# Performance work log

Measured on AMD Instinct MI355X. Metric: run time of the kernel, lower is better.

The kernel has to match this reference:

```python
import jax, jax.numpy as jnp
import numpy as np

H = 16      # num_attention_heads
D = 128     # head_size
ROT = 32    # rotary_ndims
WIN = 256   # attention_window[layer_id]
G = 64      # max_global_tokens
BASE = 10000.0


def _rotate_half(x):
    x1, x2 = jnp.split(x, 2, axis=-1)
    return jnp.concatenate([-x2, x1], axis=-1)


def setup_inputs() -> dict:
    key = jax.random.key(0)
    ks = jax.random.split(key, 6)
    B, S, HD = 2, 2048, H * D
    hidden_states = jax.random.normal(ks[0], (B, S, HD), jnp.float32)
    attention_mask = jnp.zeros((B, 1, 1, S), jnp.float32)
    glob_idx = jnp.sort(jax.random.randint(ks[1], (B, G), 0, S), axis=-1)
    W_qkv = jax.random.normal(ks[2], (HD, 3 * HD), jnp.float32) * 0.02
    b_qkv = jnp.zeros((3 * HD,), jnp.float32)
    W_o = jax.random.normal(ks[3], (HD, HD), jnp.float32) * 0.02
    b_o = jnp.zeros((HD,), jnp.float32)
    return {"hidden_states": hidden_states, "attention_mask": attention_mask,
            "glob_idx": glob_idx, "W_qkv": W_qkv, "b_qkv": b_qkv,
            "W_o": W_o, "b_o": b_o}


def reference(hidden_states, attention_mask, glob_idx, W_qkv, b_qkv, W_o, b_o):
    B, S, HD = hidden_states.shape
    qkv = (hidden_states @ W_qkv + b_qkv).reshape(B, S, H, 3 * D)
    q = qkv[..., :D].transpose(0, 2, 1, 3)        # [B,H,S,D]
    k = qkv[..., D:2 * D].transpose(0, 2, 1, 3)
    v = qkv[..., 2 * D:].transpose(0, 2, 1, 3)

    # GPT-NeoX rotary on first ROT dims
    inv_freq = 1.0 / (BASE ** (jnp.arange(0, ROT, 2, dtype=jnp.float32) / ROT))
    freqs = jnp.einsum('s,f->sf', jnp.arange(S, dtype=jnp.float32), inv_freq)
    emb = jnp.concatenate([freqs, freqs], axis=-1)           # [S,ROT]
    cos = jnp.cos(emb)[None, None]
    sin = jnp.sin(emb)[None, None]
    q = jnp.concatenate([q[..., :ROT] * cos + _rotate_half(q[..., :ROT]) * sin,
                         q[..., ROT:]], axis=-1)
    k = jnp.concatenate([k[..., :ROT] * cos + _rotate_half(k[..., :ROT]) * sin,
                         k[..., ROT:]], axis=-1)

    # step_attn path: keys/values are head-averaged before attention (key.mean(1))
    k_mean = k.mean(axis=1)   # [B,S,D]
    v_mean = v.mean(axis=1)
    scale = 1.0 / jnp.sqrt(jnp.float32(D))
    minv = jnp.finfo(jnp.float32).min

    s0 = jnp.einsum('bhqd,bkd->bhqk', q[:, :, :WIN], k_mean[:, :WIN]) * scale
    causal = jnp.tril(jnp.ones((WIN, WIN), bool))
    s0 = jnp.where(causal[None, None], s0, minv) + attention_mask[..., :WIN]
    out0 = jnp.einsum('bhqk,bkd->bhqd', jax.nn.softmax(s0, axis=-1), v_mean[:, :WIN])

    Sq = S - WIN
    steps = jnp.arange(Sq)
    win_pos = steps[:, None] + 1 + jnp.arange(WIN)[None, :]
    k_win = k_mean[:, win_pos]
    v_win = v_mean[:, win_pos]
    mask_win = attention_mask[:, 0, 0, :][:, win_pos][:, None]
    qs = q[:, :, WIN:]                                        # [B,H,Sq,D]
    s_win = jnp.einsum('bhqd,bqwd->bhqw', qs, k_win) * scale + mask_win

    k_glob = jnp.take_along_axis(k_mean, glob_idx[..., None], axis=1)  # [B,G,D]
    v_glob = jnp.take_along_axis(v_mean, glob_idx[..., None], axis=1)
    # sorted indices: 'filter < i then truncate to G' == prefix-valid mask per slot
    valid = (glob_idx[:, None, :] < steps[None, :, None])[:, None]     # [B,1,Sq,G]
    s_glob = jnp.where(valid, jnp.einsum('bhqd,bgd->bhqg', qs, k_glob) * scale, minv)

    w = jax.nn.softmax(jnp.concatenate([s_glob, s_win], axis=-1), axis=-1)
    out_steps = (jnp.einsum('bhqg,bgd->bhqd', w[..., :G], v_glob)
                 + jnp.einsum('bhqw,bqwd->bhqd', w[..., G:], v_win))

    out = jnp.concatenate([out0, out_steps], axis=2)          # [B,H,S,D]
    out = out.transpose(0, 2, 1, 3).reshape(B, S, HD)
    return out @ W_o + b_o
```

## Files before the change

### kernel.cpp

```cpp
#include <hip/hip_runtime.h>
#include <math.h>

#define SCALE_ 0.08838834764831845f
#define MINV_  (-3.4028234663852886e38f)

typedef __bf16 bf16;
typedef bf16  bf16x4 __attribute__((ext_vector_type(4)));
typedef bf16  bf16x8 __attribute__((ext_vector_type(8)));
typedef float f32x4  __attribute__((ext_vector_type(4)));
typedef float f32x16 __attribute__((ext_vector_type(16)));
typedef float float4v __attribute__((ext_vector_type(4)));

#define LD8(p) (*(const bf16x8*)(p))

__device__ __forceinline__ f32x4 mfma16(bf16x8 a, bf16x8 b, f32x4 c) {
    return __builtin_amdgcn_mfma_f32_16x16x32_bf16(a, b, c, 0, 0, 0);
}
__device__ __forceinline__ f32x16 mfma32(bf16x8 a, bf16x8 b, f32x16 c) {
    return __builtin_amdgcn_mfma_f32_32x32x16_bf16(a, b, c, 0, 0, 0);
}

typedef const __attribute__((address_space(1))) void* gas_t;
typedef __attribute__((address_space(3))) void* sas_t;
__device__ __forceinline__ void gload_lds16(const void* g, void* l) {
    __builtin_amdgcn_global_load_lds((gas_t)g, (sas_t)l, 16, 0, 0);
}


__global__ __launch_bounds__(256) void cast_hidden_kernel(const float* __restrict__ X, bf16* __restrict__ Y)
{
    int i = (blockIdx.x * 256 + threadIdx.x) * 4;
    float4v v = *(const float4v*)(X + i);
    bf16x4 o; o.x = (bf16)v.x; o.y = (bf16)v.y; o.z = (bf16)v.z; o.w = (bf16)v.w;
    *(bf16x4*)(Y + i) = o;
}

__global__ __launch_bounds__(256) void transpose_cast_kernel(const float* __restrict__ W, bf16* __restrict__ BT,
                                                             int srcStride, int qmap)
{
    __shared__ float tile[32][33];
    int k0 = blockIdx.x * 32, n0 = blockIdx.y * 32;
    int c = threadIdx.x & 31, r = threadIdx.x >> 5;
    int n = n0 + c;
    int src = qmap ? ((n >> 7) * 384 + (n & 127)) : n;
    #pragma unroll
    for (int rr = 0; rr < 32; rr += 8)
        tile[r + rr][c] = W[(size_t)(k0 + r + rr) * srcStride + src];
    __syncthreads();
    #pragma unroll
    for (int rr = 0; rr < 32; rr += 8)
        BT[(size_t)(n0 + r + rr) * 2048 + k0 + c] = (bf16)tile[c][r + rr];
}

__global__ __launch_bounds__(256) void bt1_kv_kernel(const float* __restrict__ Wqkv, bf16* __restrict__ BT1)
{
    int k0 = blockIdx.x * 16;
    int j = threadIdx.x;
    float acc[16];
    #pragma unroll
    for (int k = 0; k < 16; k++) acc[k] = 0.f;
    for (int h = 0; h < 16; h++) {
        #pragma unroll
        for (int k = 0; k < 16; k++)
            acc[k] += Wqkv[(size_t)(k0 + k) * 6144 + h * 384 + 128 + j];
    }
    #pragma unroll
    for (int k = 0; k < 16; k++)
        BT1[(size_t)(2048 + j) * 2048 + k0 + k] = (bf16)(acc[k] * 0.0625f);
}

__global__ void bias1_kernel(const float* __restrict__ bqkv, float* __restrict__ bias1)
{
    int c = blockIdx.x * 256 + threadIdx.x;
    if (c >= 2304) return;
    if (c < 2048) bias1[c] = bqkv[(c >> 7) * 384 + (c & 127)];
    else {
        int j = c - 2048; float s = 0.f;
        for (int h = 0; h < 16; h++) s += bqkv[h * 384 + 128 + j];
        bias1[c] = s * 0.0625f;
    }
}

template<int OUT_BF16>
__global__ __launch_bounds__(256) void gemm_kernel(const bf16* __restrict__ A, const bf16* __restrict__ BT,
                                                   const float* __restrict__ bias, void* __restrict__ Cout,
                                                   int M, int N, int K)
{
    __shared__ __align__(16) bf16 As[128 * 64];
    __shared__ __align__(16) bf16 Bs[128 * 64];
    const int tid  = threadIdx.x;
    const int wv   = tid >> 6, lane = tid & 63, l32 = lane & 31, half = lane >> 5;
    const int wrow = wv >> 1, wcol = wv & 1;
    const int m0 = blockIdx.y * 128, n0 = blockIdx.x * 128;

    int rowS[4], colS[4];
    #pragma unroll
    for (int j = 0; j < 4; j++) {
        int flat = (wv * 4 + j) * 64 + lane;
        int row = flat >> 3, cp = flat & 7;
        rowS[j] = row;
        colS[j] = (cp ^ (row & 7)) * 8;
    }

    f32x16 acc[2][2];
    #pragma unroll
    for (int i = 0; i < 2; i++)
        #pragma unroll
        for (int j = 0; j < 2; j++)
            #pragma unroll
            for (int r = 0; r < 16; r++) acc[i][j][r] = 0.f;

    for (int kk = 0; kk < K; kk += 64) {
        __syncthreads();
        #pragma unroll
        for (int j = 0; j < 4; j++) {
            gload_lds16(A  + (size_t)(m0 + rowS[j]) * K + kk + colS[j], &As[(wv * 4 + j) * 512]);
            gload_lds16(BT + (size_t)(n0 + rowS[j]) * K + kk + colS[j], &Bs[(wv * 4 + j) * 512]);
        }
        __syncthreads();

        bf16x8 af[2][4], bfr[2][4];
        #pragma unroll
        for (int mt = 0; mt < 2; mt++) {
            int row = wrow * 64 + mt * 32 + l32;
            #pragma unroll
            for (int k16 = 0; k16 < 4; k16++) {
                int lc = k16 * 2 + half;
                af[mt][k16] = LD8(&As[row * 64 + ((lc ^ (row & 7)) * 8)]);
            }
        }
        #pragma unroll
        for (int nt = 0; nt < 2; nt++) {
            int row = wcol * 64 + nt * 32 + l32;
            #pragma unroll
            for (int k16 = 0; k16 < 4; k16++) {
                int lc = k16 * 2 + half;
                bfr[nt][k16] = LD8(&Bs[row * 64 + ((lc ^ (row & 7)) * 8)]);
            }
        }
        #pragma unroll
        for (int k16 = 0; k16 < 4; k16++)
            #pragma unroll
            for (int mt = 0; mt < 2; mt++)
                #pragma unroll
                for (int nt = 0; nt < 2; nt++)
                    acc[mt][nt] = mfma32(af[mt][k16], bfr[nt][k16], acc[mt][nt]);
    }

    #pragma unroll
    for (int mt = 0; mt < 2; mt++) {
        #pragma unroll
        for (int nt = 0; nt < 2; nt++) {
            int n = n0 + wcol * 64 + nt * 32 + l32;
            float bn = bias[n];
            #pragma unroll
            for (int r = 0; r < 16; r++) {
                int m = m0 + wrow * 64 + mt * 32 + (r & 3) + 8 * (r >> 2) + 4 * half;
                float v = acc[mt][nt][r] + bn;
                if (OUT_BF16) ((bf16*)Cout)[(size_t)m * N + n] = (bf16)v;
                else          ((float*)Cout)[(size_t)m * N + n] = v;
            }
        }
    }
}

__global__ __launch_bounds__(320) void rotary_kernel(bf16* __restrict__ C1)
{
    int row = blockIdx.x;
    int s = row & 2047;
    int t = threadIdx.x;
    if (t >= 272) return;
    int g = t >> 4, dd = t & 15;
    bf16* ptr = C1 + (size_t)row * 2304 + (g < 16 ? g * 128 : 2048);
    float x0 = (float)ptr[dd], x1 = (float)ptr[dd + 16];
    const float L = 0.575646273248511f;
    float inv = __expf(-L * (float)dd);
    float ang = (float)s * inv;
    float c, si;
    __sincosf(ang, &si, &c);
    ptr[dd]      = (bf16)(x0 * c - x1 * si);
    ptr[dd + 16] = (bf16)(x1 * c + x0 * si);
}

__global__ __launch_bounds__(256) void build_vmT_kernel(const bf16* __restrict__ C1, bf16* __restrict__ vmT)
{
    __shared__ float tile[32][33];
    int b = blockIdx.z;
    int s0 = blockIdx.x * 32, d0 = blockIdx.y * 32;
    int c = threadIdx.x & 31, r = threadIdx.x >> 5;
    #pragma unroll
    for (int rr = 0; rr < 32; rr += 8)
        tile[r + rr][c] = (float)C1[(size_t)(b * 2048 + s0 + r + rr) * 2304 + 2176 + d0 + c];
    __syncthreads();
    #pragma unroll
    for (int rr = 0; rr < 32; rr += 8)
        vmT[(size_t)(b * 128 + d0 + r + rr) * 2048 + s0 + c] = (bf16)tile[c][r + rr];
}

__global__ __launch_bounds__(256) void pretile_kernel(const bf16* __restrict__ C1, const bf16* __restrict__ vmT,
                                                      const int* __restrict__ gidx,
                                                      bf16* __restrict__ KF, bf16* __restrict__ VF)
{
    int c = blockIdx.x, b = blockIdx.y;
    bool isGlob = (c == 32);
    for (int i = 0; i < 8; i++) {
        int sid = threadIdx.x + i * 256;
        int lane = sid & 63, fi = (sid >> 6) & 15;
        int l16 = lane & 15, quad = lane >> 4;
        if (sid < 1024) {
            int t = fi >> 2, ks = fi & 3;
            int pos = isGlob ? gidx[b * 64 + t * 16 + l16] : (c * 64 + t * 16 + l16);
            const bf16* src = C1 + (size_t)(b * 2048 + pos) * 2304 + 2048 + ks * 32 + quad * 8;
            *(bf16x8*)&KF[((size_t)(b * 33 + c) * 16 + fi) * 512 + lane * 8] = LD8(src);
        } else {
            int dt = fi >> 1, ks2 = fi & 1;
            int d = dt * 16 + l16;
            if (isGlob) {
                bf16 tmp[8];
                #pragma unroll
                for (int j = 0; j < 8; j++) {
                    int pos = gidx[b * 64 + ks2 * 32 + quad * 8 + j];
                    tmp[j] = vmT[(size_t)(b * 128 + d) * 2048 + pos];
                }
                #pragma unroll
                for (int j = 0; j < 8; j++)
                    VF[((size_t)(b * 33 + 32) * 16 + fi) * 512 + lane * 8 + j] = tmp[j];
            } else {
                const bf16* src = vmT + (size_t)(b * 128 + d) * 2048 + c * 64 + ks2 * 32 + quad * 8;
                *(bf16x8*)&VF[((size_t)(b * 33 + c) * 16 + fi) * 512 + lane * 8] = LD8(src);
            }
        }
    }
}

#define PSTRIDE 88

__global__ __launch_bounds__(256) void attn0_kernel(const bf16* __restrict__ C1, const bf16* __restrict__ KF,
                                                    const bf16* __restrict__ VF, const float* __restrict__ mask,
                                                    bf16* __restrict__ attn)
{
    const int bx = blockIdx.x, h = blockIdx.y, b = blockIdx.z;
    const int tid = threadIdx.x, wv = tid >> 6, lane = tid & 63, quad = lane >> 4, l16 = lane & 15;
    const int q0 = (bx * 4 + wv) * 16;

    __shared__ __align__(16) bf16 Ps[4 * 16 * PSTRIDE];
    bf16* Pw = &Ps[wv * (16 * PSTRIDE)];

    bf16x8 af[4];
    const bf16* qbase = C1 + (size_t)(b * 2048 + q0 + l16) * 2304 + h * 128;
    #pragma unroll
    for (int ks = 0; ks < 4; ks++) af[ks] = LD8(qbase + ks * 32 + quad * 8);

    f32x4 m_run = (f32x4){MINV_, MINV_, MINV_, MINV_};
    f32x4 l_run = (f32x4){0.f, 0.f, 0.f, 0.f};
    f32x4 O[8];
    #pragma unroll
    for (int dt = 0; dt < 8; dt++) O[dt] = (f32x4){0.f, 0.f, 0.f, 0.f};

    for (int c = 0; c <= bx; c++) {
        const bf16* KFc = KF + ((size_t)(b * 33 + c) * 16) * 512;
        const bf16* VFc = VF + ((size_t)(b * 33 + c) * 16) * 512;

        f32x4 acc[4];
        #pragma unroll
        for (int t = 0; t < 4; t++) acc[t] = (f32x4){0.f, 0.f, 0.f, 0.f};
        #pragma unroll
        for (int t = 0; t < 4; t++)
            #pragma unroll
            for (int ks = 0; ks < 4; ks++)
                acc[t] = mfma16(af[ks], LD8(KFc + (size_t)(t * 4 + ks) * 512 + lane * 8), acc[t]);

        float sv[4][4];
        #pragma unroll
        for (int t = 0; t < 4; t++) {
            int key = c * 64 + t * 16 + l16;
            float addv = mask[b * 2048 + key];
            #pragma unroll
            for (int r = 0; r < 4; r++) {
                int q = q0 + quad * 4 + r;
                sv[t][r] = (key <= q) ? (acc[t][r] * SCALE_ + addv) : MINV_;
            }
        }

        f32x4 cm;
        #pragma unroll
        for (int r = 0; r < 4; r++) cm[r] = fmaxf(fmaxf(sv[0][r], sv[1][r]), fmaxf(sv[2][r], sv[3][r]));
        #pragma unroll
        for (int ms = 1; ms < 16; ms <<= 1)
            #pragma unroll
            for (int r = 0; r < 4; r++) cm[r] = fmaxf(cm[r], __shfl_xor(cm[r], ms, 64));

        f32x4 nm, alpha;
        #pragma unroll
        for (int r = 0; r < 4; r++) { nm[r] = fmaxf(m_run[r], cm[r]); alpha[r] = __expf(m_run[r] - nm[r]); }

        float pv[4][4];
        f32x4 cs = (f32x4){0.f, 0.f, 0.f, 0.f};
        #pragma unroll
        for (int t = 0; t < 4; t++)
            #pragma unroll
            for (int r = 0; r < 4; r++) {
                pv[t][r] = __expf(sv[t][r] - nm[r]);
                cs[r] += pv[t][r];
            }
        #pragma unroll
        for (int ms = 1; ms < 16; ms <<= 1)
            #pragma unroll
            for (int r = 0; r < 4; r++) cs[r] += __shfl_xor(cs[r], ms, 64);

        m_run = nm;
        #pragma unroll
        for (int r = 0; r < 4; r++) l_run[r] = l_run[r] * alpha[r] + cs[r];
        #pragma unroll
        for (int dt = 0; dt < 8; dt++)
            #pragma unroll
            for (int r = 0; r < 4; r++) O[dt][r] *= alpha[r];

        #pragma unroll
        for (int t = 0; t < 4; t++)
            #pragma unroll
            for (int r = 0; r < 4; r++)
                Pw[(quad * 4 + r) * PSTRIDE + t * 16 + l16] = (bf16)pv[t][r];
        bf16x8 pa0 = LD8(&Pw[l16 * PSTRIDE + quad * 8]);
        bf16x8 pa1 = LD8(&Pw[l16 * PSTRIDE + 32 + quad * 8]);

        #pragma unroll
        for (int dt = 0; dt < 8; dt++) {
            O[dt] = mfma16(pa0, LD8(VFc + (size_t)(dt * 2 + 0) * 512 + lane * 8), O[dt]);
            O[dt] = mfma16(pa1, LD8(VFc + (size_t)(dt * 2 + 1) * 512 + lane * 8), O[dt]);
        }
    }

    f32x4 invl;
    #pragma unroll
    for (int r = 0; r < 4; r++) invl[r] = 1.0f / l_run[r];
    #pragma unroll
    for (int dt = 0; dt < 8; dt++)
        #pragma unroll
        for (int r = 0; r < 4; r++) {
            int q = q0 + quad * 4 + r;
            attn[(size_t)(b * 2048 + q) * 2048 + h * 128 + dt * 16 + l16] = (bf16)(O[dt][r] * invl[r]);
        }
}

__global__ __launch_bounds__(256) void attn_steps3_kernel(const bf16* __restrict__ C1, const bf16* __restrict__ KF,
                                                          const bf16* __restrict__ VF, const float* __restrict__ mask,
                                                          const int* __restrict__ gidx, bf16* __restrict__ attn)
{
    const int sb = blockIdx.x, b = blockIdx.y;
    const int tid = threadIdx.x, wv = tid >> 6, lane = tid & 63, quad = lane >> 4, l16 = lane & 15;
    const int step = sb * 4 + wv, p = 256 + step;

    __shared__ __align__(16) bf16 Ps[4 * 16 * PSTRIDE];
    bf16* Pw = &Ps[wv * (16 * PSTRIDE)];

    bf16x8 af[4];
    const bf16* qrow = C1 + (size_t)(b * 2048 + p) * 2304;
    #pragma unroll
    for (int ks = 0; ks < 4; ks++) af[ks] = LD8(qrow + l16 * 128 + ks * 32 + quad * 8);

    int gix[4];
    #pragma unroll
    for (int t = 0; t < 4; t++) gix[t] = gidx[b * 64 + t * 16 + l16];

    f32x4 m_run = (f32x4){MINV_, MINV_, MINV_, MINV_};
    f32x4 l_run = (f32x4){0.f, 0.f, 0.f, 0.f};
    f32x4 O[8];
    #pragma unroll
    for (int dt = 0; dt < 8; dt++) O[dt] = (f32x4){0.f, 0.f, 0.f, 0.f};

    const int c0 = (step + 1) >> 6;

    for (int iter = 0; iter < 6; iter++) {
        int c;
        bool isGlob = (iter == 0);
        if (isGlob) c = 32;
        else { c = c0 + iter - 1; if (c > 31) break; }

        const bf16* KFc = KF + ((size_t)(b * 33 + c) * 16) * 512;
        const bf16* VFc = VF + ((size_t)(b * 33 + c) * 16) * 512;

        f32x4 acc[4];
        #pragma unroll
        for (int t = 0; t < 4; t++) acc[t] = (f32x4){0.f, 0.f, 0.f, 0.f};
        #pragma unroll
        for (int t = 0; t < 4; t++)
            #pragma unroll
            for (int ks = 0; ks < 4; ks++)
                acc[t] = mfma16(af[ks], LD8(KFc + (size_t)(t * 4 + ks) * 512 + lane * 8), acc[t]);

        float sv[4][4];
        bool vld[4];
        #pragma unroll
        for (int t = 0; t < 4; t++) {
            float addv = 0.f;
            if (isGlob) vld[t] = gix[t] < step;
            else {
                int pos = c * 64 + t * 16 + l16;
                vld[t] = (unsigned)(pos - step - 1) < 256u;
                addv = mask[b * 2048 + pos];
            }
            #pragma unroll
            for (int r = 0; r < 4; r++) sv[t][r] = vld[t] ? (acc[t][r] * SCALE_ + addv) : MINV_;
        }

        f32x4 cm;
        #pragma unroll
        for (int r = 0; r < 4; r++) cm[r] = fmaxf(fmaxf(sv[0][r], sv[1][r]), fmaxf(sv[2][r], sv[3][r]));
        #pragma unroll
        for (int ms = 1; ms < 16; ms <<= 1)
            #pragma unroll
            for (int r = 0; r < 4; r++) cm[r] = fmaxf(cm[r], __shfl_xor(cm[r], ms, 64));

        f32x4 nm, alpha;
        #pragma unroll
        for (int r = 0; r < 4; r++) { nm[r] = fmaxf(m_run[r], cm[r]); alpha[r] = __expf(m_run[r] - nm[r]); }

        float pv[4][4];
        f32x4 cs = (f32x4){0.f, 0.f, 0.f, 0.f};
        #pragma unroll
        for (int t = 0; t < 4; t++)
            #pragma unroll
            for (int r = 0; r < 4; r++) {
                pv[t][r] = vld[t] ? __expf(sv[t][r] - nm[r]) : 0.f;
                cs[r] += pv[t][r];
            }
        #pragma unroll
        for (int ms = 1; ms < 16; ms <<= 1)
            #pragma unroll
            for (int r = 0; r < 4; r++) cs[r] += __shfl_xor(cs[r], ms, 64);

        m_run = nm;
        #pragma unroll
        for (int r = 0; r < 4; r++) l_run[r] = l_run[r] * alpha[r] + cs[r];
        #pragma unroll
        for (int dt = 0; dt < 8; dt++)
            #pragma unroll
            for (int r = 0; r < 4; r++) O[dt][r] *= alpha[r];

        #pragma unroll
        for (int t = 0; t < 4; t++)
            #pragma unroll
            for (int r = 0; r < 4; r++)
                Pw[(quad * 4 + r) * PSTRIDE + t * 16 + l16] = (bf16)pv[t][r];
        bf16x8 pa0 = LD8(&Pw[l16 * PSTRIDE + quad * 8]);
        bf16x8 pa1 = LD8(&Pw[l16 * PSTRIDE + 32 + quad * 8]);

        #pragma unroll
        for (int dt = 0; dt < 8; dt++) {
            O[dt] = mfma16(pa0, LD8(VFc + (size_t)(dt * 2 + 0) * 512 + lane * 8), O[dt]);
            O[dt] = mfma16(pa1, LD8(VFc + (size_t)(dt * 2 + 1) * 512 + lane * 8), O[dt]);
        }
    }

    f32x4 invl;
    #pragma unroll
    for (int r = 0; r < 4; r++) invl[r] = 1.0f / l_run[r];
    #pragma unroll
    for (int dt = 0; dt < 8; dt++)
        #pragma unroll
        for (int r = 0; r < 4; r++) {
            int h = quad * 4 + r;
            attn[(size_t)(b * 2048 + p) * 2048 + h * 128 + dt * 16 + l16] = (bf16)(O[dt][r] * invl[r]);
        }
}

extern "C" void kernel_launch(void* const* d_in, const int* in_sizes, int n_in,
                              void* d_out, int out_size, void* d_ws, size_t ws_size,
                              hipStream_t stream)
{
    const float* hidden = (const float*)d_in[0];
    const float* amask  = (const float*)d_in[1];
    const int*   gidx   = (const int*)d_in[2];
    const float* Wqkv   = (const float*)d_in[3];
    const float* bqkv   = (const float*)d_in[4];
    const float* Wo     = (const float*)d_in[5];
    const float* bo     = (const float*)d_in[6];

    char* ws = (char*)d_ws;
    size_t off = 0;
    auto take = [&](size_t bytes) -> char* {
        char* p = ws + off;
        off = (off + bytes + 255) & ~(size_t)255;
        return p;
    };
    bf16*  A16   = (bf16*)take(4096ull * 2048 * 2);
    bf16*  BT1   = (bf16*)take(2304ull * 2048 * 2);
    bf16*  BT2   = (bf16*)take(2048ull * 2048 * 2);
    bf16*  C1    = (bf16*)take(4096ull * 2304 * 2);
    bf16*  vmT   = (bf16*)take(2ull * 128 * 2048 * 2);
    bf16*  KF    = (bf16*)take(2ull * 33 * 16 * 512 * 2);
    bf16*  VF    = (bf16*)take(2ull * 33 * 16 * 512 * 2);
    bf16*  attnb = (bf16*)take(4096ull * 2048 * 2);
    float* bias1 = (float*)take(2304 * 4);

    cast_hidden_kernel<<<8192, 256, 0, stream>>>(hidden, A16);
    transpose_cast_kernel<<<dim3(64, 64), 256, 0, stream>>>(Wqkv, BT1, 6144, 1);
    bt1_kv_kernel<<<128, 256, 0, stream>>>(Wqkv, BT1);
    bias1_kernel<<<9, 256, 0, stream>>>(bqkv, bias1);
    transpose_cast_kernel<<<dim3(64, 64), 256, 0, stream>>>(Wo, BT2, 2048, 0);

    gemm_kernel<1><<<dim3(18, 32), 256, 0, stream>>>(A16, BT1, bias1, (void*)C1, 4096, 2304, 2048);

    rotary_kernel<<<4096, 320, 0, stream>>>(C1);
    build_vmT_kernel<<<dim3(64, 4, 2), 256, 0, stream>>>(C1, vmT);
    pretile_kernel<<<dim3(33, 2), 256, 0, stream>>>(C1, vmT, gidx, KF, VF);

    attn0_kernel<<<dim3(4, 16, 2), 256, 0, stream>>>(C1, KF, VF, amask, attnb);
    attn_steps3_kernel<<<dim3(448, 2), 256, 0, stream>>>(C1, KF, VF, amask, gidx, attnb);

    gemm_kernel<0><<<dim3(16, 32), 256, 0, stream>>>(attnb, BT2, bo, d_out, 4096, 2048, 2048);

    (void)in_sizes; (void)n_in; (void)out_size; (void)ws_size;
}
```

Before: 320.7 us.

## Double-buffer GEMM, fuse rotary into epilogue, merge setup and attention launches

The GEMM gets two LDS buffers and prefetches two K-tiles ahead, using explicit vmcnt waits and barriers. It also remaps workgroups in XCD-interleaved order and raises wave priority around the MFMAs. Rotary embedding moves into the QKV GEMM epilogue, using a lane shuffle to pair dims d and d+16, which removes a separate read-modify-write pass over C1. The two weight transposes, the bias setup and the two attention kernels are each merged into single launches to cut launch count and tail idle time. The risks are doubled LDS use lowering occupancy and the hand-placed waitcnt counts being fragile.

Result: slower. 335.0 us (+4.5%).

```diff
diff --git a/kernel.cpp b/kernel.cpp
--- a/kernel.cpp
+++ b/kernel.cpp
@@ -35,14 +35,18 @@
     *(bf16x4*)(Y + i) = o;
 }
 
-__global__ __launch_bounds__(256) void transpose_cast_kernel(const float* __restrict__ W, bf16* __restrict__ BT,
-                                                             int srcStride, int qmap)
+__global__ __launch_bounds__(256) void transpose_cast2_kernel(const float* __restrict__ Wqkv, bf16* __restrict__ BT1,
+                                                              const float* __restrict__ Wo, bf16* __restrict__ BT2)
 {
     __shared__ float tile[32][33];
+    int z = blockIdx.z;
+    const float* W = z ? Wo : Wqkv;
+    bf16* BT = z ? BT2 : BT1;
+    int srcStride = z ? 2048 : 6144;
     int k0 = blockIdx.x * 32, n0 = blockIdx.y * 32;
     int c = threadIdx.x & 31, r = threadIdx.x >> 5;
     int n = n0 + c;
-    int src = qmap ? ((n >> 7) * 384 + (n & 127)) : n;
+    int src = z ? n : ((n >> 7) * 384 + (n & 127));
     #pragma unroll
     for (int rr = 0; rr < 32; rr += 8)
         tile[r + rr][c] = W[(size_t)(k0 + r + rr) * srcStride + src];
@@ -52,8 +56,20 @@
         BT[(size_t)(n0 + r + rr) * 2048 + k0 + c] = (bf16)tile[c][r + rr];
 }
 
-__global__ __launch_bounds__(256) void bt1_kv_kernel(const float* __restrict__ Wqkv, bf16* __restrict__ BT1)
-{
+__global__ __launch_bounds__(256) void bt1_kv_kernel(const float* __restrict__ Wqkv, const float* __restrict__ bqkv,
+                                                     bf16* __restrict__ BT1, float* __restrict__ bias1)
+{
+    if (blockIdx.x == 128) {
+        for (int c = threadIdx.x; c < 2304; c += 256) {
+            if (c < 2048) bias1[c] = bqkv[(c >> 7) * 384 + (c & 127)];
+            else {
+                int j = c - 2048; float s = 0.f;
+                for (int h = 0; h < 16; h++) s += bqkv[h * 384 + 128 + j];
+                bias1[c] = s * 0.0625f;
+            }
+        }
+        return;
+    }
     int k0 = blockIdx.x * 16;
     int j = threadIdx.x;
     float acc[16];
@@ -69,29 +85,26 @@
         BT1[(size_t)(2048 + j) * 2048 + k0 + k] = (bf16)(acc[k] * 0.0625f);
 }
 
-__global__ void bias1_kernel(const float* __restrict__ bqkv, float* __restrict__ bias1)
-{
-    int c = blockIdx.x * 256 + threadIdx.x;
-    if (c >= 2304) return;
-    if (c < 2048) bias1[c] = bqkv[(c >> 7) * 384 + (c & 127)];
-    else {
-        int j = c - 2048; float s = 0.f;
-        for (int h = 0; h < 16; h++) s += bqkv[h * 384 + 128 + j];
-        bias1[c] = s * 0.0625f;
-    }
-}
-
-template<int OUT_BF16>
+template<int OUT_BF16, int ROTARY>
 __global__ __launch_bounds__(256) void gemm_kernel(const bf16* __restrict__ A, const bf16* __restrict__ BT,
                                                    const float* __restrict__ bias, void* __restrict__ Cout,
                                                    int M, int N, int K)
 {
-    __shared__ __align__(16) bf16 As[128 * 64];
-    __shared__ __align__(16) bf16 Bs[128 * 64];
+    __shared__ __align__(16) bf16 As[2][128 * 64];
+    __shared__ __align__(16) bf16 Bs[2][128 * 64];
     const int tid  = threadIdx.x;
     const int wv   = tid >> 6, lane = tid & 63, l32 = lane & 31, half = lane >> 5;
     const int wrow = wv >> 1, wcol = wv & 1;
-    const int m0 = blockIdx.y * 128, n0 = blockIdx.x * 128;
+
+    const int gx = gridDim.x;
+    const int nwg = gx * gridDim.y;
+    int orig = blockIdx.y * gx + blockIdx.x;
+    int wgid = orig;
+    if ((nwg & 7) == 0) {
+        int cpx = nwg >> 3;
+        wgid = (orig & 7) * cpx + (orig >> 3);
+    }
+    const int m0 = (wgid / gx) * 128, n0 = (wgid % gx) * 128;
 
     int rowS[4], colS[4];
     #pragma unroll
@@ -102,6 +115,17 @@
         colS[j] = (cp ^ (row & 7)) * 8;
     }
 
+    const int nt = K >> 6;
+
+    auto stage = [&](int t, int b) {
+        int kk = t << 6;
+        #pragma unroll
+        for (int j = 0; j < 4; j++) {
+            gload_lds16(A  + (size_t)(m0 + rowS[j]) * K + kk + colS[j], &As[b][(wv * 4 + j) * 512]);
+            gload_lds16(BT + (size_t)(n0 + rowS[j]) * K + kk + colS[j], &Bs[b][(wv * 4 + j) * 512]);
+        }
+    };
+
     f32x16 acc[2][2];
     #pragma unroll
     for (int i = 0; i < 2; i++)
@@ -110,15 +134,18 @@
             #pragma unroll
             for (int r = 0; r < 16; r++) acc[i][j][r] = 0.f;
 
-    for (int kk = 0; kk < K; kk += 64) {
-        __syncthreads();
-        #pragma unroll
-        for (int j = 0; j < 4; j++) {
-            gload_lds16(A  + (size_t)(m0 + rowS[j]) * K + kk + colS[j], &As[(wv * 4 + j) * 512]);
-            gload_lds16(BT + (size_t)(n0 + rowS[j]) * K + kk + colS[j], &Bs[(wv * 4 + j) * 512]);
-        }
-        __syncthreads();
-
+    stage(0, 0);
+    stage(1, 1);
+
+    for (int t = 0; t < nt; ++t) {
+        const int cur = t & 1;
+        if (t < nt - 1) asm volatile("s_waitcnt vmcnt(8)" ::: "memory");
+        else            asm volatile("s_waitcnt vmcnt(0)" ::: "memory");
+        __builtin_amdgcn_s_barrier();
+        asm volatile("" ::: "memory");
+
+        const bf16* Ab = &As[cur][0];
+        const bf16* Bb = &Bs[cur][0];
         bf16x8 af[2][4], bfr[2][4];
         #pragma unroll
         for (int mt = 0; mt < 2; mt++) {
@@ -126,60 +153,64 @@
             #pragma unroll
             for (int k16 = 0; k16 < 4; k16++) {
                 int lc = k16 * 2 + half;
-                af[mt][k16] = LD8(&As[row * 64 + ((lc ^ (row & 7)) * 8)]);
-            }
-        }
-        #pragma unroll
-        for (int nt = 0; nt < 2; nt++) {
-            int row = wcol * 64 + nt * 32 + l32;
+                af[mt][k16] = LD8(&Ab[row * 64 + ((lc ^ (row & 7)) * 8)]);
+            }
+        }
+        #pragma unroll
+        for (int ntt = 0; ntt < 2; ntt++) {
+            int row = wcol * 64 + ntt * 32 + l32;
             #pragma unroll
             for (int k16 = 0; k16 < 4; k16++) {
                 int lc = k16 * 2 + half;
-                bfr[nt][k16] = LD8(&Bs[row * 64 + ((lc ^ (row & 7)) * 8)]);
-            }
-        }
+                bfr[ntt][k16] = LD8(&Bb[row * 64 + ((lc ^ (row & 7)) * 8)]);
+            }
+        }
+        __builtin_amdgcn_s_setprio(1);
         #pragma unroll
         for (int k16 = 0; k16 < 4; k16++)
             #pragma unroll
             for (int mt = 0; mt < 2; mt++)
                 #pragma unroll
-                for (int nt = 0; nt < 2; nt++)
-                    acc[mt][nt] = mfma32(af[mt][k16], bfr[nt][k16], acc[mt][nt]);
+                for (int ntt = 0; ntt < 2; ntt++)
+                    acc[mt][ntt] = mfma32(af[mt][k16], bfr[ntt][k16], acc[mt][ntt]);
+        __builtin_amdgcn_s_setprio(0);
+
+        asm volatile("" ::: "memory");
+        __builtin_amdgcn_s_barrier();
+        asm volatile("" ::: "memory");
+        if (t + 2 < nt) stage(t + 2, cur);
     }
 
     #pragma unroll
     for (int mt = 0; mt < 2; mt++) {
         #pragma unroll
-        for (int nt = 0; nt < 2; nt++) {
-            int n = n0 + wcol * 64 + nt * 32 + l32;
+        for (int ntt = 0; ntt < 2; ntt++) {
+            int n = n0 + wcol * 64 + ntt * 32 + l32;
             float bn = bias[n];
+            float vv[16];
+            #pragma unroll
+            for (int r = 0; r < 16; r++) vv[r] = acc[mt][ntt][r] + bn;
+            if (ROTARY && wcol == 0 && ntt == 0 && n0 <= 2048) {
+                const float L = 0.575646273248511f;
+                float inv = __expf(-L * (float)(l32 & 15));
+                #pragma unroll
+                for (int r = 0; r < 16; r++) {
+                    int m = m0 + wrow * 64 + mt * 32 + (r & 3) + 8 * (r >> 2) + 4 * half;
+                    float ang = (float)(m & 2047) * inv;
+                    float cs, sn;
+                    __sincosf(ang, &sn, &cs);
+                    float pv = __shfl_xor(vv[r], 16, 64);
+                    vv[r] = (l32 < 16) ? (vv[r] * cs - pv * sn) : (vv[r] * cs + pv * sn);
+                }
+            }
             #pragma unroll
             for (int r = 0; r < 16; r++) {
                 int m = m0 + wrow * 64 + mt * 32 + (r & 3) + 8 * (r >> 2) + 4 * half;
-                float v = acc[mt][nt][r] + bn;
-                if (OUT_BF16) ((bf16*)Cout)[(size_t)m * N + n] = (bf16)v;
-                else          ((float*)Cout)[(size_t)m * N + n] = v;
-            }
-        }
-    }
-}
-
-__global__ __launch_bounds__(320) void rotary_kernel(bf16* __restrict__ C1)
-{
-    int row = blockIdx.x;
-    int s = row & 2047;
-    int t = threadIdx.x;
-    if (t >= 272) return;
-    int g = t >> 4, dd = t & 15;
-    bf16* ptr = C1 + (size_t)row * 2304 + (g < 16 ? g * 128 : 2048);
-    float x0 = (float)ptr[dd], x1 = (float)ptr[dd + 16];
-    const float L = 0.575646273248511f;
-    float inv = __expf(-L * (float)dd);
-    float ang = (float)s * inv;
-    float c, si;
-    __sincosf(ang, &si, &c);
-    ptr[dd]      = (bf16)(x0 * c - x1 * si);
-    ptr[dd + 16] = (bf16)(x1 * c + x0 * si);
+                if (OUT_BF16) ((bf16*)Cout)[(size_t)m * N + n] = (bf16)vv[r];
+                else          ((float*)Cout)[(size_t)m * N + n] = vv[r];
+            }
+        }
+    }
 }
 
 __global__ __launch_bounds__(256) void build_vmT_kernel(const bf16* __restrict__ C1, bf16* __restrict__ vmT)
@@ -235,16 +266,13 @@
 
 #define PSTRIDE 88
 
-__global__ __launch_bounds__(256) void attn0_kernel(const bf16* __restrict__ C1, const bf16* __restrict__ KF,
-                                                    const bf16* __restrict__ VF, const float* __restrict__ mask,
-                                                    bf16* __restrict__ attn)
-{
-    const int bx = blockIdx.x, h = blockIdx.y, b = blockIdx.z;
+__device__ __forceinline__ void attn0_body(int bx, int h, int b, bf16* Pw,
+                                           const bf16* __restrict__ C1, const bf16* __restrict__ KF,
+                                           const bf16* __restrict__ VF, const float* __restrict__ mask,
+                                           bf16* __restrict__ attn)
+{
     const int tid = threadIdx.x, wv = tid >> 6, lane = tid & 63, quad = lane >> 4, l16 = lane & 15;
     const int q0 = (bx * 4 + wv) * 16;
-
-    __shared__ __align__(16) bf16 Ps[4 * 16 * PSTRIDE];
-    bf16* Pw = &Ps[wv * (16 * PSTRIDE)];
 
     bf16x8 af[4];
     const bf16* qbase = C1 + (size_t)(b * 2048 + q0 + l16) * 2304 + h * 128;
@@ -343,16 +371,13 @@
         }
 }
 
-__global__ __launch_bounds__(256) void attn_steps3_kernel(const bf16* __restrict__ C1, const bf16* __restrict__ KF,
-                                                          const bf16* __restrict__ VF, const float* __restrict__ mask,
-                                                          const int* __restrict__ gidx, bf16* __restrict__ attn)
-{
-    const int sb = blockIdx.x, b = blockIdx.y;
+__device__ __forceinline__ void attn_steps_body(int sb, int b, bf16* Pw,
+                                                const bf16* __restrict__ C1, const bf16* __restrict__ KF,
+                                                const bf16* __restrict__ VF, const float* __restrict__ mask,
+                                                const int* __restrict__ gidx, bf16* __restrict__ attn)
+{
     const int tid = threadIdx.x, wv = tid >> 6, lane = tid & 63, quad = lane >> 4, l16 = lane & 15;
     const int step = sb * 4 + wv, p = 256 + step;
-
-    __shared__ __align__(16) bf16 Ps[4 * 16 * PSTRIDE];
-    bf16* Pw = &Ps[wv * (16 * PSTRIDE)];
 
     bf16x8 af[4];
     const bf16* qrow = C1 + (size_t)(b * 2048 + p) * 2304;
@@ -463,6 +488,21 @@
             int h = quad * 4 + r;
             attn[(size_t)(b * 2048 + p) * 2048 + h * 128 + dt * 16 + l16] = (bf16)(O[dt][r] * invl[r]);
         }
+}
+
+__global__ __launch_bounds__(256) void attn_all_kernel(const bf16* __restrict__ C1, const bf16* __restrict__ KF,
+                                                       const bf16* __restrict__ VF, const float* __restrict__ mask,
+                                                       const int* __restrict__ gidx, bf16* __restrict__ attn)
+{
+    __shared__ __align__(16) bf16 Ps[4 * 16 * PSTRIDE];
+    const int wv = threadIdx.x >> 6;
+    bf16* Pw = &Ps[wv * (16 * PSTRIDE)];
+    if (blockIdx.x < 448) {
+        attn_steps_body(blockIdx.x, blockIdx.y, Pw, C1, KF, VF, mask, gidx, attn);
+    } else {
+        int bi = blockIdx.x - 448;
+        attn0_body(bi >> 4, bi & 15, blockIdx.y, Pw, C1, KF, VF, mask, attn);
+    }
 }
 
 extern "C" void kernel_launch(void* const* d_in, const int* in_sizes, int n_in,
@@ -495,21 +535,17 @@
     float* bias1 = (float*)take(2304 * 4);
 
     cast_hidden_kernel<<<8192, 256, 0, stream>>>(hidden, A16);
-    transpose_cast_kernel<<<dim3(64, 64), 256, 0, stream>>>(Wqkv, BT1, 6144, 1);
-    bt1_kv_kernel<<<128, 256, 0, stream>>>(Wqkv, BT1);
-    bias1_kernel<<<9, 256, 0, stream>>>(bqkv, bias1);
-    transpose_cast_kernel<<<dim3(64, 64), 256, 0, stream>>>(Wo, BT2, 2048, 0);
-
-    gemm_kernel<1><<<dim3(18, 32), 256, 0, stream>>>(A16, BT1, bias1, (void*)C1, 4096, 2304, 2048);
-
-    rotary_kernel<<<4096, 320, 0, stream>>>(C1);
+    transpose_cast2_kernel<<<dim3(64, 64, 2), 256, 0, stream>>>(Wqkv, BT1, Wo, BT2);
+    bt1_kv_kernel<<<129, 256, 0, stream>>>(Wqkv, bqkv, BT1, bias1);
+
+    gemm_kernel<1, 1><<<dim3(18, 32), 256, 0, stream>>>(A16, BT1, bias1, (void*)C1, 4096, 2304, 2048);
+
     build_vmT_kernel<<<dim3(64, 4, 2), 256, 0, stream>>>(C1, vmT);
     pretile_kernel<<<dim3(33, 2), 256, 0, stream>>>(C1, vmT, gidx, KF, VF);
 
-    attn0_kernel<<<dim3(4, 16, 2), 256, 0, stream>>>(C1, KF, VF, amask, attnb);
-    attn_steps3_kernel<<<dim3(448, 2), 256, 0, stream>>>(C1, KF, VF, amask, gidx, attnb);
-
-    gemm_kernel<0><<<dim3(16, 32), 256, 0, stream>>>(attnb, BT2, bo, d_out, 4096, 2048, 2048);
+    attn_all_kernel<<<dim3(512, 2), 256, 0, stream>>>(C1, KF, VF, amask, gidx, attnb);
+
+    gemm_kernel<0, 0><<<dim3(16, 32), 256, 0, stream>>>(attnb, BT2, bo, d_out, 4096, 2048, 2048);
 
     (void)in_sizes; (void)n_in; (void)out_size; (void)ws_size;
 }
```
